# Performance work log

Measured on AMD Instinct MI355X. Metric: run time of the kernel, lower is better.

Reference implementation:

```python
import jax, jax.numpy as jnp
import numpy as np

FANOUT = 10
NT = [61952, 5632, 512]      # targets produced by layer i
NN = [681472, 61952, 5632]   # input nodes consumed by layer i
NE = [619520, 56320, 5120]   # sampled edges for layer i (NT[i]*FANOUT)
IN_DIM = 256
HID = 256
NCLS = 47
EPS = 1e-5


def setup_inputs() -> dict:
    key = jax.random.key(0)
    ks = jax.random.split(key, 16)
    inp = {}
    inp['x_feat'] = jax.random.normal(ks[0], (NN[0], IN_DIM), jnp.float32)
    for i in range(3):
        # each target samples exactly FANOUT neighbors -> dst is repeat(arange)
        inp[f'src{i}'] = jax.random.randint(ks[1 + i], (NE[i],), 0, NN[i], dtype=jnp.int32)
        inp[f'dst{i}'] = jnp.repeat(jnp.arange(NT[i], dtype=jnp.int32), FANOUT)
        inp[f'tlid{i}'] = jax.random.randint(ks[4 + i], (NT[i],), 0, NN[i], dtype=jnp.int32)
        d_in = IN_DIM if i == 0 else HID
        s = 1.0 / np.sqrt(d_in)
        inp[f'Wl{i}'] = jax.random.uniform(ks[7 + i], (d_in, HID), jnp.float32, -s, s)
        inp[f'Wr{i}'] = jax.random.uniform(ks[10 + i], (d_in, HID), jnp.float32, -s, s)
        inp[f'b{i}'] = jnp.zeros((HID,), jnp.float32)
        inp[f'g{i}'] = jnp.ones((HID,), jnp.float32)
        inp[f'be{i}'] = jnp.zeros((HID,), jnp.float32)
    sf = 1.0 / np.sqrt(HID)
    inp['fc_w'] = jax.random.uniform(ks[13], (HID, NCLS), jnp.float32, -sf, sf)
    inp['fc_b'] = jnp.zeros((NCLS,), jnp.float32)
    return inp


def _sage_bn_relu(x, src, dst, tlid, Wl, Wr, b, g, be, n_t):
    # gather neighbor messages and mean-aggregate per target (SAGEConv, mean aggr)
    msg = x[src]                                               # [E, d_in]
    agg = jax.ops.segment_sum(msg, dst, num_segments=n_t)      # [T, d_in]
    cnt = jax.ops.segment_sum(jnp.ones(src.shape, x.dtype), dst, num_segments=n_t)
    agg = agg / jnp.maximum(cnt, 1.0)[:, None]
    x_tgt = x[tlid]                                            # F.embedding gather of target feats
    h = agg @ Wl + x_tgt @ Wr + b                              # lin_l(agg) + lin_r(x_target)
    # BatchNorm1d in training mode (biased batch stats)
    mu = h.mean(axis=0)
    var = h.var(axis=0)
    h = (h - mu) * jax.lax.rsqrt(var + EPS) * g + be
    return jax.nn.relu(h)


def reference(x_feat, src0, dst0, tlid0, src1, dst1, tlid1, src2, dst2, tlid2,
              Wl0, Wr0, b0, g0, be0, Wl1, Wr1, b1, g1, be1, Wl2, Wr2, b2, g2, be2,
              fc_w, fc_b):
    x = x_feat
    layers = [
        (src0, dst0, tlid0, Wl0, Wr0, b0, g0, be0, NT[0]),
        (src1, dst1, tlid1, Wl1, Wr1, b1, g1, be1, NT[1]),
        (src2, dst2, tlid2, Wl2, Wr2, b2, g2, be2, NT[2]),
    ]
    for (src, dst, tlid, Wl, Wr, b, g, be, n_t) in layers:
        x = _sage_bn_relu(x, src, dst, tlid, Wl, Wr, b, g, be, n_t)
    out = x @ fc_w + fc_b                                      # [B, class_count]
    return out
```

## Files before the change

kernel.cpp:

```cpp
#include <hip/hip_runtime.h>

#define HID 256
#define FANOUT 10

typedef __attribute__((ext_vector_type(8))) short bf16x8;
typedef __attribute__((ext_vector_type(4))) float f32x4;

__device__ __forceinline__ unsigned short f2bf(float f) {
    unsigned int u = __float_as_uint(f);
    u += 0x7FFFu + ((u >> 16) & 1u);
    return (unsigned short)(u >> 16);
}

__device__ __forceinline__ void gld_lds16(const void* g, void* l) {
    __builtin_amdgcn_global_load_lds((const __attribute__((address_space(1))) void*)g,
                                     (__attribute__((address_space(3))) void*)l, 16, 0, 0);
}

__global__ __launch_bounds__(256)
void agg_gather_kernel(const float* __restrict__ x, const int* __restrict__ src,
                       const int* __restrict__ tlid, unsigned short* __restrict__ Ag,
                       int T) {
    const int wave = threadIdx.x >> 6, lane = threadIdx.x & 63;
    const int t = blockIdx.x * 4 + wave;
    if (t >= T) return;
    const float4* x4 = (const float4*)x;
    const int* sp = src + (size_t)t * FANOUT;
    float sx = 0.f, sy = 0.f, sz = 0.f, sw = 0.f;
#pragma unroll
    for (int j = 0; j < FANOUT; ++j) {
        const float4 v = x4[(size_t)sp[j] * 64 + lane];
        sx += v.x; sy += v.y; sz += v.z; sw += v.w;
    }
    const float4 tv = x4[(size_t)tlid[t] * 64 + lane];

    const int rb = t >> 6;
    const int i  = (t & 63) >> 4;
    const int m0 = t & 15;
    const int cl   = lane >> 3;
    const int quad = (lane >> 1) & 3;
    const int j0   = (lane & 1) * 4;
    const int lf   = quad * 16 + m0;
    const size_t base = (size_t)rb * 32768 + (size_t)i * 512 + (size_t)lf * 8 + j0;

    ushort4 oa, ot;
    oa.x = f2bf(sx * 0.1f); oa.y = f2bf(sy * 0.1f);
    oa.z = f2bf(sz * 0.1f); oa.w = f2bf(sw * 0.1f);
    ot.x = f2bf(tv.x); ot.y = f2bf(tv.y); ot.z = f2bf(tv.z); ot.w = f2bf(tv.w);
    *(ushort4*)&Ag[base + (size_t)cl * 2048]       = oa;
    *(ushort4*)&Ag[base + (size_t)(cl + 8) * 2048] = ot;
}

__global__ __launch_bounds__(256)
void convw_kernel(const float* __restrict__ Wl, const float* __restrict__ Wr,
                  unsigned short* __restrict__ Wt) {
    const int idx = blockIdx.x * 256 + threadIdx.x;
    const int kc = idx & 31, n = (idx >> 5) & 255, c = idx >> 13;
    const int k = c * 32 + kc;
    const float v = (k < 256) ? Wl[k * 256 + n] : Wr[(k - 256) * 256 + n];
    Wt[idx] = f2bf(v);
}

__global__ __launch_bounds__(256)
void gemm_mfma_kernel(const unsigned short* __restrict__ Ag,
                      const unsigned short* __restrict__ Wt,
                      const float* __restrict__ bias,
                      float* __restrict__ hbuf) {
    __shared__ unsigned short Alds[2048];
    __shared__ unsigned short Blds[8192];
    const int tid = threadIdx.x, wave = tid >> 6, lane = tid & 63;
    const size_t rb = blockIdx.x;

    f32x4 acc[4][4];
#pragma unroll
    for (int a = 0; a < 4; ++a)
#pragma unroll
        for (int b = 0; b < 4; ++b) acc[a][b] = (f32x4){0.f, 0.f, 0.f, 0.f};

    const unsigned short* Abase = Ag + rb * 32768;
    const int soff = wave * 512 + lane * 8;

    for (int c = 0; c < 16; ++c) {
        __syncthreads();
        gld_lds16(Abase + (size_t)c * 2048 + soff, &Alds[wave * 512]);
        const unsigned short* Bb = Wt + (size_t)c * 8192;
#pragma unroll
        for (int ii = 0; ii < 4; ++ii)
            gld_lds16(Bb + ii * 2048 + soff, &Blds[ii * 2048 + wave * 512]);
        __syncthreads();

        bf16x8 af[4], bfr[4];
#pragma unroll
        for (int mi = 0; mi < 4; ++mi)
            af[mi] = *(const bf16x8*)&Alds[(mi * 64 + lane) * 8];
        const int nb = wave * 64 + (lane & 15);
        const int ko = (lane >> 4) * 8;
#pragma unroll
        for (int t = 0; t < 4; ++t)
            bfr[t] = *(const bf16x8*)&Blds[(nb + t * 16) * 32 + ko];

#pragma unroll
        for (int mi = 0; mi < 4; ++mi)
#pragma unroll
            for (int t = 0; t < 4; ++t)
                acc[mi][t] = __builtin_amdgcn_mfma_f32_16x16x32_bf16(
                    af[mi], bfr[t], acc[mi][t], 0, 0, 0);
    }

    const int q = lane >> 4, m0 = lane & 15;
#pragma unroll
    for (int t = 0; t < 4; ++t) {
        const int col = wave * 64 + t * 16 + m0;
        const float bv = bias[col];
#pragma unroll
        for (int mi = 0; mi < 4; ++mi) {
            float* op = hbuf + (rb * 64 + (size_t)mi * 16 + q * 4) * 256 + col;
#pragma unroll
            for (int r = 0; r < 4; ++r)
                op[(size_t)r * 256] = acc[mi][t][r] + bv;
        }
    }
}

__global__ void zero_kernel(float* p) { p[threadIdx.x] = 0.f; }

__global__ __launch_bounds__(256)
void stats_kernel(const float* __restrict__ h, float* __restrict__ ssum,
                  float* __restrict__ ssq, int T) {
    const int c = threadIdx.x;
    float s = 0.f, q = 0.f;
    for (int r = blockIdx.x; r < T; r += gridDim.x) {
        const float v = h[(size_t)r * HID + c];
        s += v;
        q += v * v;
    }
    atomicAdd(&ssum[c], s);
    atomicAdd(&ssq[c], q);
}

__global__ void bnfin_kernel(const float* __restrict__ ssum, const float* __restrict__ ssq,
                             const float* __restrict__ g, const float* __restrict__ be,
                             float* __restrict__ scal, float* __restrict__ shft,
                             float invT) {
    const int c = threadIdx.x;
    const float mu = ssum[c] * invT;
    float var = ssq[c] * invT - mu * mu;
    var = fmaxf(var, 0.f);
    const float rs = rsqrtf(var + 1e-5f);
    const float sc = rs * g[c];
    scal[c] = sc;
    shft[c] = be[c] - mu * sc;
}

__global__ __launch_bounds__(256)
void norm_kernel(float* __restrict__ h, const float* __restrict__ scal,
                 const float* __restrict__ shft, int n4) {
    const int i = blockIdx.x * blockDim.x + threadIdx.x;
    if (i >= n4) return;
    const int c4 = i & 63;
    float4 v = ((float4*)h)[i];
    const float4 sc = ((const float4*)scal)[c4];
    const float4 sh = ((const float4*)shft)[c4];
    v.x = fmaxf(fmaf(v.x, sc.x, sh.x), 0.f);
    v.y = fmaxf(fmaf(v.y, sc.y, sh.y), 0.f);
    v.z = fmaxf(fmaf(v.z, sc.z, sh.z), 0.f);
    v.w = fmaxf(fmaf(v.w, sc.w, sh.w), 0.f);
    ((float4*)h)[i] = v;
}

__global__ __launch_bounds__(64)
void fc_kernel(const float* __restrict__ x, const float* __restrict__ w,
               const float* __restrict__ b, float* __restrict__ out, int C) {
    __shared__ float row[HID];
    const int r = blockIdx.x;
    const int tid = threadIdx.x;
    ((float4*)row)[tid] = ((const float4*)(x + (size_t)r * HID))[tid];
    __syncthreads();
    if (tid < C) {
        float acc = b[tid];
#pragma unroll 8
        for (int k = 0; k < HID; ++k)
            acc = fmaf(row[k], w[k * C + tid], acc);
        out[(size_t)r * C + tid] = acc;
    }
}

extern "C" void kernel_launch(void* const* d_in, const int* in_sizes, int n_in,
                              void* d_out, int out_size, void* d_ws, size_t ws_size,
                              hipStream_t stream) {
    const float* x_feat = (const float*)d_in[0];
    const int T0 = in_sizes[3];
    const int T1 = in_sizes[11];
    const int T2 = in_sizes[19];
    const int NCLS = in_sizes[26];

    float* buf0 = (float*)d_ws;
    float* buf1 = buf0 + (size_t)T0 * HID;
    float* buf2 = buf1 + (size_t)T1 * HID;
    float* ssum = buf2 + (size_t)T2 * HID;
    float* ssq  = ssum + HID;
    float* scal = ssq + HID;
    float* shft = scal + HID;
    unsigned short* Wt = (unsigned short*)(shft + HID + 256);
    unsigned short* Ag = Wt + 512 * 256;

    const float* xs[3]   = { x_feat, buf0, buf1 };
    float*       bufs[3] = { buf0, buf1, buf2 };
    const int    Ts[3]   = { T0, T1, T2 };

    for (int i = 0; i < 3; ++i) {
        const int base = 1 + i * 8;
        const int*   src  = (const int*)d_in[base + 0];
        const int*   tlid = (const int*)d_in[base + 2];
        const float* Wl   = (const float*)d_in[base + 3];
        const float* Wr   = (const float*)d_in[base + 4];
        const float* bi   = (const float*)d_in[base + 5];
        const float* g    = (const float*)d_in[base + 6];
        const float* be   = (const float*)d_in[base + 7];
        const int T = Ts[i];

        convw_kernel<<<512, 256, 0, stream>>>(Wl, Wr, Wt);
        agg_gather_kernel<<<(T + 3) / 4, 256, 0, stream>>>(xs[i], src, tlid, Ag, T);
        zero_kernel<<<1, 512, 0, stream>>>(ssum);
        gemm_mfma_kernel<<<T / 64, 256, 0, stream>>>(Ag, Wt, bi, bufs[i]);
        int sg = T / 64;
        if (sg > 256) sg = 256;
        if (sg < 1) sg = 1;
        stats_kernel<<<sg, 256, 0, stream>>>(bufs[i], ssum, ssq, T);
        bnfin_kernel<<<1, HID, 0, stream>>>(ssum, ssq, g, be, scal, shft, 1.0f / (float)T);
        norm_kernel<<<(T * 64 + 255) / 256, 256, 0, stream>>>(bufs[i], scal, shft, T * 64);
    }

    const float* fc_w = (const float*)d_in[25];
    const float* fc_b = (const float*)d_in[26];
    fc_kernel<<<T2, 64, 0, stream>>>(buf2, fc_w, fc_b, (float*)d_out, NCLS);
}
```

Baseline: 1.152 ms.

## Fuse BN stats into GEMM epilogue and BN-apply into next gather

Computes per-column sum and sum of squares in the GEMM epilogue via shuffles and atomics, removing the separate stats pass. The BN scale/shift and ReLU are applied on the fly in the next layer's gather and in the FC kernel, removing the standalone normalize pass over the hidden buffer. The bias add is dropped because batch norm cancels it. All three weight conversions are done in one launch up front. This trades extra atomics contention on 256 addresses for eliminating full read/write sweeps of the large layer outputs.

```diff
diff --git a/kernel.cpp b/kernel.cpp
--- a/kernel.cpp
+++ b/kernel.cpp
@@ -20,19 +20,38 @@
 __global__ __launch_bounds__(256)
 void agg_gather_kernel(const float* __restrict__ x, const int* __restrict__ src,
                        const int* __restrict__ tlid, unsigned short* __restrict__ Ag,
-                       int T) {
+                       int T, const float* __restrict__ scal,
+                       const float* __restrict__ shft, int apply) {
     const int wave = threadIdx.x >> 6, lane = threadIdx.x & 63;
     const int t = blockIdx.x * 4 + wave;
     if (t >= T) return;
     const float4* x4 = (const float4*)x;
+    float4 sc = make_float4(1.f, 1.f, 1.f, 1.f);
+    float4 sh = make_float4(0.f, 0.f, 0.f, 0.f);
+    if (apply) {
+        sc = ((const float4*)scal)[lane];
+        sh = ((const float4*)shft)[lane];
+    }
     const int* sp = src + (size_t)t * FANOUT;
     float sx = 0.f, sy = 0.f, sz = 0.f, sw = 0.f;
 #pragma unroll
     for (int j = 0; j < FANOUT; ++j) {
-        const float4 v = x4[(size_t)sp[j] * 64 + lane];
+        float4 v = x4[(size_t)sp[j] * 64 + lane];
+        if (apply) {
+            v.x = fmaxf(fmaf(v.x, sc.x, sh.x), 0.f);
+            v.y = fmaxf(fmaf(v.y, sc.y, sh.y), 0.f);
+            v.z = fmaxf(fmaf(v.z, sc.z, sh.z), 0.f);
+            v.w = fmaxf(fmaf(v.w, sc.w, sh.w), 0.f);
+        }
         sx += v.x; sy += v.y; sz += v.z; sw += v.w;
     }
-    const float4 tv = x4[(size_t)tlid[t] * 64 + lane];
+    float4 tv = x4[(size_t)tlid[t] * 64 + lane];
+    if (apply) {
+        tv.x = fmaxf(fmaf(tv.x, sc.x, sh.x), 0.f);
+        tv.y = fmaxf(fmaf(tv.y, sc.y, sh.y), 0.f);
+        tv.z = fmaxf(fmaf(tv.z, sc.z, sh.z), 0.f);
+        tv.w = fmaxf(fmaf(tv.w, sc.w, sh.w), 0.f);
+    }
 
     const int rb = t >> 6;
     const int i  = (t & 63) >> 4;
@@ -52,10 +71,15 @@
 }
 
 __global__ __launch_bounds__(256)
-void convw_kernel(const float* __restrict__ Wl, const float* __restrict__ Wr,
-                  unsigned short* __restrict__ Wt) {
+void convw_all_kernel(const float* __restrict__ Wl0, const float* __restrict__ Wr0,
+                      const float* __restrict__ Wl1, const float* __restrict__ Wr1,
+                      const float* __restrict__ Wl2, const float* __restrict__ Wr2,
+                      unsigned short* __restrict__ Wt) {
     const int idx = blockIdx.x * 256 + threadIdx.x;
-    const int kc = idx & 31, n = (idx >> 5) & 255, c = idx >> 13;
+    const int layer = idx >> 17, r = idx & 131071;
+    const float* Wl = (layer == 0) ? Wl0 : (layer == 1) ? Wl1 : Wl2;
+    const float* Wr = (layer == 0) ? Wr0 : (layer == 1) ? Wr1 : Wr2;
+    const int kc = r & 31, n = (r >> 5) & 255, c = r >> 13;
     const int k = c * 32 + kc;
     const float v = (k < 256) ? Wl[k * 256 + n] : Wr[(k - 256) * 256 + n];
     Wt[idx] = f2bf(v);
@@ -64,8 +88,8 @@
 __global__ __launch_bounds__(256)
 void gemm_mfma_kernel(const unsigned short* __restrict__ Ag,
                       const unsigned short* __restrict__ Wt,
-                      const float* __restrict__ bias,
-                      float* __restrict__ hbuf) {
+                      float* __restrict__ hbuf,
+                      float* __restrict__ ssum, float* __restrict__ ssq) {
     __shared__ unsigned short Alds[2048];
     __shared__ unsigned short Blds[8192];
     const int tid = threadIdx.x, wave = tid >> 6, lane = tid & 63;
@@ -108,35 +132,48 @@
     }
 
     const int q = lane >> 4, m0 = lane & 15;
+
 #pragma unroll
     for (int t = 0; t < 4; ++t) {
         const int col = wave * 64 + t * 16 + m0;
-        const float bv = bias[col];
 #pragma unroll
         for (int mi = 0; mi < 4; ++mi) {
             float* op = hbuf + (rb * 64 + (size_t)mi * 16 + q * 4) * 256 + col;
 #pragma unroll
             for (int r = 0; r < 4; ++r)
-                op[(size_t)r * 256] = acc[mi][t][r] + bv;
+                op[(size_t)r * 256] = acc[mi][t][r];
         }
     }
+
+    float s[4], sq[4];
+#pragma unroll
+    for (int t = 0; t < 4; ++t) {
+        float a = 0.f, b = 0.f;
+#pragma unroll
+        for (int mi = 0; mi < 4; ++mi)
+#pragma unroll
+            for (int r = 0; r < 4; ++r) {
+                const float v = acc[mi][t][r];
+                a += v; b += v * v;
+            }
+        s[t] = a; sq[t] = b;
+    }
+#pragma unroll
+    for (int t = 0; t < 4; ++t) {
+        s[t] += __shfl_xor(s[t], 16);  s[t] += __shfl_xor(s[t], 32);
+        sq[t] += __shfl_xor(sq[t], 16); sq[t] += __shfl_xor(sq[t], 32);
+    }
+    if (lane < 16) {
+#pragma unroll
+        for (int t = 0; t < 4; ++t) {
+            const int col = wave * 64 + t * 16 + m0;
+            atomicAdd(&ssum[col], s[t]);
+            atomicAdd(&ssq[col], sq[t]);
+        }
+    }
 }
 
 __global__ void zero_kernel(float* p) { p[threadIdx.x] = 0.f; }
-
-__global__ __launch_bounds__(256)
-void stats_kernel(const float* __restrict__ h, float* __restrict__ ssum,
-                  float* __restrict__ ssq, int T) {
-    const int c = threadIdx.x;
-    float s = 0.f, q = 0.f;
-    for (int r = blockIdx.x; r < T; r += gridDim.x) {
-        const float v = h[(size_t)r * HID + c];
-        s += v;
-        q += v * v;
-    }
-    atomicAdd(&ssum[c], s);
-    atomicAdd(&ssq[c], q);
-}
 
 __global__ void bnfin_kernel(const float* __restrict__ ssum, const float* __restrict__ ssq,
                              const float* __restrict__ g, const float* __restrict__ be,
@@ -152,29 +189,21 @@
     shft[c] = be[c] - mu * sc;
 }
 
-__global__ __launch_bounds__(256)
-void norm_kernel(float* __restrict__ h, const float* __restrict__ scal,
-                 const float* __restrict__ shft, int n4) {
-    const int i = blockIdx.x * blockDim.x + threadIdx.x;
-    if (i >= n4) return;
-    const int c4 = i & 63;
-    float4 v = ((float4*)h)[i];
-    const float4 sc = ((const float4*)scal)[c4];
-    const float4 sh = ((const float4*)shft)[c4];
+__global__ __launch_bounds__(64)
+void fc_kernel(const float* __restrict__ x, const float* __restrict__ scal,
+               const float* __restrict__ shft, const float* __restrict__ w,
+               const float* __restrict__ b, float* __restrict__ out, int C) {
+    __shared__ float row[HID];
+    const int r = blockIdx.x;
+    const int tid = threadIdx.x;
+    float4 v = ((const float4*)(x + (size_t)r * HID))[tid];
+    const float4 sc = ((const float4*)scal)[tid];
+    const float4 sh = ((const float4*)shft)[tid];
     v.x = fmaxf(fmaf(v.x, sc.x, sh.x), 0.f);
     v.y = fmaxf(fmaf(v.y, sc.y, sh.y), 0.f);
     v.z = fmaxf(fmaf(v.z, sc.z, sh.z), 0.f);
     v.w = fmaxf(fmaf(v.w, sc.w, sh.w), 0.f);
-    ((float4*)h)[i] = v;
-}
-
-__global__ __launch_bounds__(64)
-void fc_kernel(const float* __restrict__ x, const float* __restrict__ w,
-               const float* __restrict__ b, float* __restrict__ out, int C) {
-    __shared__ float row[HID];
-    const int r = blockIdx.x;
-    const int tid = threadIdx.x;
-    ((float4*)row)[tid] = ((const float4*)(x + (size_t)r * HID))[tid];
+    ((float4*)row)[tid] = v;
     __syncthreads();
     if (tid < C) {
         float acc = b[tid];
@@ -202,36 +231,34 @@
     float* scal = ssq + HID;
     float* shft = scal + HID;
     unsigned short* Wt = (unsigned short*)(shft + HID + 256);
-    unsigned short* Ag = Wt + 512 * 256;
+    unsigned short* Ag = Wt + 3 * 512 * 256;
 
     const float* xs[3]   = { x_feat, buf0, buf1 };
     float*       bufs[3] = { buf0, buf1, buf2 };
     const int    Ts[3]   = { T0, T1, T2 };
+
+    convw_all_kernel<<<1536, 256, 0, stream>>>(
+        (const float*)d_in[4],  (const float*)d_in[5],
+        (const float*)d_in[12], (const float*)d_in[13],
+        (const float*)d_in[20], (const float*)d_in[21], Wt);
 
     for (int i = 0; i < 3; ++i) {
         const int base = 1 + i * 8;
         const int*   src  = (const int*)d_in[base + 0];
         const int*   tlid = (const int*)d_in[base + 2];
-        const float* Wl   = (const float*)d_in[base + 3];
-        const float* Wr   = (const float*)d_in[base + 4];
-        const float* bi   = (const float*)d_in[base + 5];
         const float* g    = (const float*)d_in[base + 6];
         const float* be   = (const float*)d_in[base + 7];
         const int T = Ts[i];
 
-        convw_kernel<<<512, 256, 0, stream>>>(Wl, Wr, Wt);
-        agg_gather_kernel<<<(T + 3) / 4, 256, 0, stream>>>(xs[i], src, tlid, Ag, T);
+        agg_gather_kernel<<<(T + 3) / 4, 256, 0, stream>>>(
+            xs[i], src, tlid, Ag, T, scal, shft, i > 0 ? 1 : 0);
         zero_kernel<<<1, 512, 0, stream>>>(ssum);
-        gemm_mfma_kernel<<<T / 64, 256, 0, stream>>>(Ag, Wt, bi, bufs[i]);
-        int sg = T / 64;
-        if (sg > 256) sg = 256;
-        if (sg < 1) sg = 1;
-        stats_kernel<<<sg, 256, 0, stream>>>(bufs[i], ssum, ssq, T);
+        gemm_mfma_kernel<<<T / 64, 256, 0, stream>>>(
+            Ag, Wt + (size_t)i * 131072, bufs[i], ssum, ssq);
         bnfin_kernel<<<1, HID, 0, stream>>>(ssum, ssq, g, be, scal, shft, 1.0f / (float)T);
-        norm_kernel<<<(T * 64 + 255) / 256, 256, 0, stream>>>(bufs[i], scal, shft, T * 64);
     }
 
     const float* fc_w = (const float*)d_in[25];
     const float* fc_b = (const float*)d_in[26];
-    fc_kernel<<<T2, 64, 0, stream>>>(buf2, fc_w, fc_b, (float*)d_out, NCLS);
-}
+    fc_kernel<<<T2, 64, 0, stream>>>(buf2, scal, shft, fc_w, fc_b, (float*)d_out, NCLS);
+}
```

Result: faster. 1.063 ms (-7.8%).
